# Kernel optimization log

Measured on AMD Instinct MI355X. Metric: run time of the kernel, lower is better.

## Reference

```python
import jax, jax.numpy as jnp
import numpy as np

N_EMBD = 1024
HEAD_SIZE = 64  # n_embd // n_head = 1024 // 16


def setup_inputs() -> dict:
    key = jax.random.key(0)
    ks = jax.random.split(key, 7)
    s = 0.02
    return {
        "x": jax.random.normal(ks[0], (8, 2048, N_EMBD), dtype=jnp.float32),
        "wq": jax.random.normal(ks[1], (N_EMBD, HEAD_SIZE), dtype=jnp.float32) * s,
        "bq": jax.random.normal(ks[2], (HEAD_SIZE,), dtype=jnp.float32) * s,
        "wk": jax.random.normal(ks[3], (N_EMBD, HEAD_SIZE), dtype=jnp.float32) * s,
        "bk": jax.random.normal(ks[4], (HEAD_SIZE,), dtype=jnp.float32) * s,
        "wv": jax.random.normal(ks[5], (N_EMBD, HEAD_SIZE), dtype=jnp.float32) * s,
        "bv": jax.random.normal(ks[6], (HEAD_SIZE,), dtype=jnp.float32) * s,
    }


def reference(x, wq, bq, wk, bk, wv, bv):
    B, T, C = x.shape
    q = x @ wq + bq  # [B,T,H]
    k = x @ wk + bk
    v = x @ wv + bv
    # NOTE: original scales by C**-0.5 where C = n_embd (full embedding dim)
    scale = jnp.asarray(C, x.dtype) ** -0.5
    att = jnp.einsum("bqh,bkh->bqk", q, k) * scale  # [B,T,T]
    causal = jnp.tril(jnp.ones((T, T), dtype=bool))
    att = jnp.where(causal, att, -jnp.inf)
    att = jax.nn.softmax(att, axis=-1)
    return jnp.einsum("bqk,bkh->bqh", att, v)  # [B,T,H]
```

## Files before the change

### kernel.cpp

```cpp
#include <hip/hip_runtime.h>
#include <hip/hip_bf16.h>

typedef short s8v __attribute__((ext_vector_type(8)));
typedef short s4v __attribute__((ext_vector_type(4)));
typedef float f4v __attribute__((ext_vector_type(4)));

#define MFMA16(a,b,c) __builtin_amdgcn_mfma_f32_16x16x32_bf16((a),(b),(c),0,0,0)

__device__ __forceinline__ short f2bf(float f) {
    __hip_bfloat16 h = __float2bfloat16(f);
    short s; __builtin_memcpy(&s, &h, 2); return s;
}
__device__ __forceinline__ float bf2f(short s) {
    unsigned int u = ((unsigned int)(unsigned short)s) << 16;
    float f; __builtin_memcpy(&f, &u, 4); return f;
}
__device__ __forceinline__ s4v cvt4(float4 a) {
    s4v r; r[0] = f2bf(a.x); r[1] = f2bf(a.y); r[2] = f2bf(a.z); r[3] = f2bf(a.w);
    return r;
}

__global__ __launch_bounds__(256) void pack_w_kernel(
    const float* __restrict__ wq, const float* __restrict__ wk,
    const float* __restrict__ wv, short* __restrict__ wpack)
{
    int fid  = blockIdx.x * 256 + threadIdx.x;
    int lane = fid & 63;
    int ks   = (fid >> 6) & 31;
    int t    = fid >> 11;
    int m3 = t >> 2, nt = t & 3;
    int col = nt * 16 + (lane & 15);
    int k0  = ks * 32 + (lane >> 4) * 8;
    const float* w = (m3 == 0) ? wq : (m3 == 1 ? wk : wv);
    float sc = (m3 == 0) ? 0.03125f : 1.0f;
    s8v frag;
#pragma unroll
    for (int j = 0; j < 8; j++) frag[j] = f2bf(w[(k0 + j) * 64 + col] * sc);
    ((s8v*)wpack)[fid] = frag;
}

__global__ __launch_bounds__(256) void qkv_kernel(
    const float* __restrict__ x, const short* __restrict__ wpack,
    const float* __restrict__ bq, const float* __restrict__ bk,
    const float* __restrict__ bv,
    short* __restrict__ qws, short* __restrict__ kws, short* __restrict__ vt)
{
    __shared__ short xl[2][32][136];

    int tid  = threadIdx.x;
    int wave = tid >> 6, lane = tid & 63;
    int quad = lane >> 4, l16 = lane & 15;
    int row0 = blockIdx.x * 32;
    const float* xbase = x + (size_t)row0 * 1024;
    const s8v* wp = (const s8v*)wpack;
    int tbase = wave * 3;

    f4v acc[2][3];
    f4v z = {0.f, 0.f, 0.f, 0.f};
#pragma unroll
    for (int rf = 0; rf < 2; rf++)
#pragma unroll
        for (int i = 0; i < 3; i++) acc[rf][i] = z;

    float4 xr[4];
#pragma unroll
    for (int i = 0; i < 4; i++) {
        int idx = i * 256 + tid;
        xr[i] = *(const float4*)(xbase + (size_t)(idx >> 5) * 1024 + (idx & 31) * 4);
    }
#pragma unroll
    for (int i = 0; i < 4; i++) {
        int idx = i * 256 + tid;
        *(s4v*)&xl[0][idx >> 5][(idx & 31) * 4] = cvt4(xr[i]);
    }
    __syncthreads();

    for (int sk = 0; sk < 8; sk++) {
        int cur = sk & 1, nxt = cur ^ 1;
        if (sk < 7) {
#pragma unroll
            for (int i = 0; i < 4; i++) {
                int idx = i * 256 + tid;
                xr[i] = *(const float4*)(xbase + (size_t)(idx >> 5) * 1024
                                         + (sk + 1) * 128 + (idx & 31) * 4);
            }
        }
#pragma unroll
        for (int ks = 0; ks < 4; ks++) {
            s8v a0 = *(const s8v*)&xl[cur][l16][ks * 32 + quad * 8];
            s8v a1 = *(const s8v*)&xl[cur][16 + l16][ks * 32 + quad * 8];
            int kg = sk * 4 + ks;
#pragma unroll
            for (int i = 0; i < 3; i++) {
                s8v bf = wp[((tbase + i) * 32 + kg) * 64 + lane];
                acc[0][i] = MFMA16(a0, bf, acc[0][i]);
                acc[1][i] = MFMA16(a1, bf, acc[1][i]);
            }
        }
        if (sk < 7) {
#pragma unroll
            for (int i = 0; i < 4; i++) {
                int idx = i * 256 + tid;
                *(s4v*)&xl[nxt][idx >> 5][(idx & 31) * 4] = cvt4(xr[i]);
            }
        }
        __syncthreads();
    }

    int b = row0 >> 11;
#pragma unroll
    for (int rf = 0; rf < 2; rf++) {
        int rowD = row0 + rf * 16 + quad * 4;
#pragma unroll
        for (int i = 0; i < 3; i++) {
            int t = tbase + i, m3 = t >> 2, nt = t & 3;
            int col = nt * 16 + l16;
            if (m3 == 0) {
                float bias = bq[col] * 0.03125f;
#pragma unroll
                for (int r = 0; r < 4; r++)
                    qws[(rowD + r) * 64 + col] = f2bf(acc[rf][i][r] + bias);
            } else if (m3 == 1) {
                float bias = bk[col];
#pragma unroll
                for (int r = 0; r < 4; r++)
                    kws[(rowD + r) * 64 + col] = f2bf(acc[rf][i][r] + bias);
            } else {
                float bias = bv[col];
                int keyb = rowD & 2047;
                s4v v4;
#pragma unroll
                for (int r = 0; r < 4; r++) v4[r] = f2bf(acc[rf][i][r] + bias);
                *(s4v*)(vt + (size_t)(b * 64 + col) * 2048 + keyb) = v4;
            }
        }
    }
}

__global__ __launch_bounds__(256) void attn_kernel(
    const short* __restrict__ qws, const short* __restrict__ kws,
    const short* __restrict__ vt, short* __restrict__ opart,
    float* __restrict__ lpart)
{
    __shared__ short Kl[64][72];
    __shared__ short Vl[64][72];
    __shared__ short Pl[4][16 * 72];

    int tid  = threadIdx.x;
    int wave = tid >> 6, lane = tid & 63;
    int quad = lane >> 4, l16 = lane & 15;
    int b = blockIdx.y;
    int u = 143 - blockIdx.x;

    int g = 0;
#pragma unroll
    for (int gg = 1; gg <= 7; gg++) if (u >= 2 * gg * (gg + 1)) g = gg;
    int rem = u - 2 * g * (g + 1);
    int qt = 4 * g + rem / (g + 1);
    int cc = rem % (g + 1);

    int q0 = qt * 64;
    int c0 = cc * 256;
    bool last = (cc == g);
    int jtN = last ? (((q0 + 63 - c0) >> 6) + 1) : 4;

    const short* qb  = qws + (size_t)b * 2048 * 64;
    const short* kb  = kws + (size_t)b * 2048 * 64;
    const short* vtb = vt  + (size_t)b * 64 * 2048;

    int qrow = q0 + wave * 16 + l16;
    s8v qf0 = *(const s8v*)(qb + qrow * 64 + quad * 8);
    s8v qf1 = *(const s8v*)(qb + qrow * 64 + 32 + quad * 8);

    s8v onef;
#pragma unroll
    for (int j = 0; j < 8; j++) onef[j] = (l16 == 0) ? (short)0x3F80 : (short)0;

    f4v o[5];
    f4v z = {0.f, 0.f, 0.f, 0.f};
#pragma unroll
    for (int nt = 0; nt < 5; nt++) o[nt] = z;

    int srow = tid >> 3;
    int sc   = (tid & 7) * 8;

    for (int t = 0; t < jtN; t++) {
        int key0 = c0 + t * 64;
        __syncthreads();
#pragma unroll
        for (int i = 0; i < 2; i++) {
            int r = srow + i * 32;
            *(s8v*)&Kl[r][sc] = *(const s8v*)(kb + (key0 + r) * 64 + sc);
            *(s8v*)&Vl[r][sc] = *(const s8v*)(vtb + (size_t)r * 2048 + key0 + sc);
        }
        __syncthreads();

        f4v s[4];
#pragma unroll
        for (int nt = 0; nt < 4; nt++) {
            s8v k0 = *(const s8v*)&Kl[nt * 16 + l16][quad * 8];
            s8v k1 = *(const s8v*)&Kl[nt * 16 + l16][32 + quad * 8];
            s[nt] = MFMA16(qf0, k0, z);
            s[nt] = MFMA16(qf1, k1, s[nt]);
        }

        if (last) {
            int rowbase = q0 + wave * 16 + quad * 4;
#pragma unroll
            for (int nt = 0; nt < 4; nt++) {
                int key = key0 + nt * 16 + l16;
#pragma unroll
                for (int r = 0; r < 4; r++)
                    if (key > rowbase + r) s[nt][r] = -1e30f;
            }
        }

        short* pw = Pl[wave];
#pragma unroll
        for (int nt = 0; nt < 4; nt++)
#pragma unroll
            for (int r = 0; r < 4; r++)
                pw[(quad * 4 + r) * 72 + nt * 16 + l16] = f2bf(__expf(s[nt][r]));
        asm volatile("s_waitcnt lgkmcnt(0)" ::: "memory");

#pragma unroll
        for (int st = 0; st < 2; st++) {
            s8v pf = *(const s8v*)(pw + l16 * 72 + st * 32 + quad * 8);
#pragma unroll
            for (int nt = 0; nt < 4; nt++) {
                s8v vf = *(const s8v*)&Vl[nt * 16 + l16][st * 32 + quad * 8];
                o[nt] = MFMA16(pf, vf, o[nt]);
            }
            o[4] = MFMA16(pf, onef, o[4]);
        }
    }

    int g0 = b * 2048 + q0 + wave * 16;
    short* op = opart + (size_t)cc * (16384 * 64);
#pragma unroll
    for (int nt = 0; nt < 4; nt++)
#pragma unroll
        for (int r = 0; r < 4; r++)
            op[(size_t)(g0 + quad * 4 + r) * 64 + nt * 16 + l16] = f2bf(o[nt][r]);
    if (l16 == 0) {
        float* lp = lpart + (size_t)cc * 16384;
#pragma unroll
        for (int r = 0; r < 4; r++) lp[g0 + quad * 4 + r] = o[4][r];
    }
}

__global__ __launch_bounds__(256) void combine_kernel(
    const short* __restrict__ opart, const float* __restrict__ lpart,
    float* __restrict__ out)
{
    int idx = blockIdx.x * 256 + threadIdx.x;
    int g = idx >> 4;
    int d = (idx & 15) * 4;
    int nc = ((g & 2047) >> 8) + 1;
    float s0 = 0.f, s1 = 0.f, s2 = 0.f, s3 = 0.f, lsum = 0.f;
    for (int c = 0; c < nc; c++) {
        short4 o4 = *(const short4*)(opart + (size_t)c * (16384 * 64) + g * 64 + d);
        s0 += bf2f(o4.x); s1 += bf2f(o4.y); s2 += bf2f(o4.z); s3 += bf2f(o4.w);
        lsum += lpart[c * 16384 + g];
    }
    float inv = 1.0f / lsum;
    float4 res = {s0 * inv, s1 * inv, s2 * inv, s3 * inv};
    *(float4*)(out + g * 64 + d) = res;
}

extern "C" void kernel_launch(void* const* d_in, const int* in_sizes, int n_in,
                              void* d_out, int out_size, void* d_ws, size_t ws_size,
                              hipStream_t stream) {
    const float* x  = (const float*)d_in[0];
    const float* wq = (const float*)d_in[1];
    const float* bq = (const float*)d_in[2];
    const float* wk = (const float*)d_in[3];
    const float* bk = (const float*)d_in[4];
    const float* wv = (const float*)d_in[5];
    const float* bv = (const float*)d_in[6];
    float* out = (float*)d_out;

    char* ws = (char*)d_ws;
    short* wpack = (short*)ws;
    short* qws   = (short*)(ws + (512u << 10));
    short* kws   = (short*)(ws + (512u << 10) + (2u << 20));
    short* vt    = (short*)(ws + (512u << 10) + (4u << 20));
    short* opart = (short*)(ws + (512u << 10) + (6u << 20));
    float* lpart = (float*)(ws + (512u << 10) + (22u << 20));

    hipLaunchKernelGGL(pack_w_kernel,  dim3(96),        dim3(256), 0, stream,
                       wq, wk, wv, wpack);
    hipLaunchKernelGGL(qkv_kernel,     dim3(512),       dim3(256), 0, stream,
                       x, wpack, bq, bk, bv, qws, kws, vt);
    hipLaunchKernelGGL(attn_kernel,    dim3(144, 8),    dim3(256), 0, stream,
                       qws, kws, vt, opart, lpart);
    hipLaunchKernelGGL(combine_kernel, dim3(1024),      dim3(256), 0, stream,
                       opart, lpart, out);
}
```

Measured before the change: 138.7 us.

## Double-buffer K/V tiles in attention and enlarge QKV projection row tiles

The attention kernel now prefetches the next K/V tile into registers while computing on the current shared-memory buffer, then writes it to a second buffer. This drops one barrier per iteration and hides global load latency. The QKV kernel moves to 512-thread blocks covering 64 rows with a narrower 64-wide k-step, so each weight fragment is reused across two row halves by different waves. The cost is more shared memory and registers, which may lower occupancy, and half as many QKV blocks.

```diff
diff --git a/kernel.cpp b/kernel.cpp
--- a/kernel.cpp
+++ b/kernel.cpp
@@ -39,21 +39,22 @@
     ((s8v*)wpack)[fid] = frag;
 }
 
-__global__ __launch_bounds__(256) void qkv_kernel(
+__global__ __launch_bounds__(512) void qkv_kernel(
     const float* __restrict__ x, const short* __restrict__ wpack,
     const float* __restrict__ bq, const float* __restrict__ bk,
     const float* __restrict__ bv,
     short* __restrict__ qws, short* __restrict__ kws, short* __restrict__ vt)
 {
-    __shared__ short xl[2][32][136];
+    __shared__ short xl[2][64][72];
 
     int tid  = threadIdx.x;
     int wave = tid >> 6, lane = tid & 63;
     int quad = lane >> 4, l16 = lane & 15;
-    int row0 = blockIdx.x * 32;
+    int row0 = blockIdx.x * 64;
+    int rhalf = (wave & 1) * 32;
+    int tbase = (wave >> 1) * 3;
     const float* xbase = x + (size_t)row0 * 1024;
     const s8v* wp = (const s8v*)wpack;
-    int tbase = wave * 3;
 
     f4v acc[2][3];
     f4v z = {0.f, 0.f, 0.f, 0.f};
@@ -62,34 +63,34 @@
 #pragma unroll
         for (int i = 0; i < 3; i++) acc[rf][i] = z;
 
-    float4 xr[4];
-#pragma unroll
-    for (int i = 0; i < 4; i++) {
-        int idx = i * 256 + tid;
-        xr[i] = *(const float4*)(xbase + (size_t)(idx >> 5) * 1024 + (idx & 31) * 4);
-    }
-#pragma unroll
-    for (int i = 0; i < 4; i++) {
-        int idx = i * 256 + tid;
-        *(s4v*)&xl[0][idx >> 5][(idx & 31) * 4] = cvt4(xr[i]);
+    float4 xr[2];
+#pragma unroll
+    for (int i = 0; i < 2; i++) {
+        int idx = i * 512 + tid;
+        xr[i] = *(const float4*)(xbase + (size_t)(idx >> 4) * 1024 + (idx & 15) * 4);
+    }
+#pragma unroll
+    for (int i = 0; i < 2; i++) {
+        int idx = i * 512 + tid;
+        *(s4v*)&xl[0][idx >> 4][(idx & 15) * 4] = cvt4(xr[i]);
     }
     __syncthreads();
 
-    for (int sk = 0; sk < 8; sk++) {
+    for (int sk = 0; sk < 16; sk++) {
         int cur = sk & 1, nxt = cur ^ 1;
-        if (sk < 7) {
-#pragma unroll
-            for (int i = 0; i < 4; i++) {
-                int idx = i * 256 + tid;
-                xr[i] = *(const float4*)(xbase + (size_t)(idx >> 5) * 1024
-                                         + (sk + 1) * 128 + (idx & 31) * 4);
-            }
-        }
-#pragma unroll
-        for (int ks = 0; ks < 4; ks++) {
-            s8v a0 = *(const s8v*)&xl[cur][l16][ks * 32 + quad * 8];
-            s8v a1 = *(const s8v*)&xl[cur][16 + l16][ks * 32 + quad * 8];
-            int kg = sk * 4 + ks;
+        if (sk < 15) {
+#pragma unroll
+            for (int i = 0; i < 2; i++) {
+                int idx = i * 512 + tid;
+                xr[i] = *(const float4*)(xbase + (size_t)(idx >> 4) * 1024
+                                         + (sk + 1) * 64 + (idx & 15) * 4);
+            }
+        }
+#pragma unroll
+        for (int ks = 0; ks < 2; ks++) {
+            s8v a0 = *(const s8v*)&xl[cur][rhalf + l16][ks * 32 + quad * 8];
+            s8v a1 = *(const s8v*)&xl[cur][rhalf + 16 + l16][ks * 32 + quad * 8];
+            int kg = sk * 2 + ks;
 #pragma unroll
             for (int i = 0; i < 3; i++) {
                 s8v bf = wp[((tbase + i) * 32 + kg) * 64 + lane];
@@ -97,20 +98,20 @@
                 acc[1][i] = MFMA16(a1, bf, acc[1][i]);
             }
         }
-        if (sk < 7) {
-#pragma unroll
-            for (int i = 0; i < 4; i++) {
-                int idx = i * 256 + tid;
-                *(s4v*)&xl[nxt][idx >> 5][(idx & 31) * 4] = cvt4(xr[i]);
-            }
-        }
-        __syncthreads();
+        if (sk < 15) {
+#pragma unroll
+            for (int i = 0; i < 2; i++) {
+                int idx = i * 512 + tid;
+                *(s4v*)&xl[nxt][idx >> 4][(idx & 15) * 4] = cvt4(xr[i]);
+            }
+            __syncthreads();
+        }
     }
 
     int b = row0 >> 11;
 #pragma unroll
     for (int rf = 0; rf < 2; rf++) {
-        int rowD = row0 + rf * 16 + quad * 4;
+        int rowD = row0 + rhalf + rf * 16 + quad * 4;
 #pragma unroll
         for (int i = 0; i < 3; i++) {
             int t = tbase + i, m3 = t >> 2, nt = t & 3;
@@ -142,8 +143,8 @@
     const short* __restrict__ vt, short* __restrict__ opart,
     float* __restrict__ lpart)
 {
-    __shared__ short Kl[64][72];
-    __shared__ short Vl[64][72];
+    __shared__ short Kl[2][64][72];
+    __shared__ short Vl[2][64][72];
     __shared__ short Pl[4][16 * 72];
 
     int tid  = threadIdx.x;
@@ -184,22 +185,41 @@
     int srow = tid >> 3;
     int sc   = (tid & 7) * 8;
 
+    s8v kr[2], vr[2];
+#pragma unroll
+    for (int i = 0; i < 2; i++) {
+        int r = srow + i * 32;
+        kr[i] = *(const s8v*)(kb + (c0 + r) * 64 + sc);
+        vr[i] = *(const s8v*)(vtb + (size_t)r * 2048 + c0 + sc);
+    }
+#pragma unroll
+    for (int i = 0; i < 2; i++) {
+        int r = srow + i * 32;
+        *(s8v*)&Kl[0][r][sc] = kr[i];
+        *(s8v*)&Vl[0][r][sc] = vr[i];
+    }
+    __syncthreads();
+
     for (int t = 0; t < jtN; t++) {
+        int cur = t & 1, nxt = cur ^ 1;
         int key0 = c0 + t * 64;
-        __syncthreads();
-#pragma unroll
-        for (int i = 0; i < 2; i++) {
-            int r = srow + i * 32;
-            *(s8v*)&Kl[r][sc] = *(const s8v*)(kb + (key0 + r) * 64 + sc);
-            *(s8v*)&Vl[r][sc] = *(const s8v*)(vtb + (size_t)r * 2048 + key0 + sc);
-        }
-        __syncthreads();
+        bool more = (t + 1 < jtN);
+
+        if (more) {
+            int key1 = key0 + 64;
+#pragma unroll
+            for (int i = 0; i < 2; i++) {
+                int r = srow + i * 32;
+                kr[i] = *(const s8v*)(kb + (key1 + r) * 64 + sc);
+                vr[i] = *(const s8v*)(vtb + (size_t)r * 2048 + key1 + sc);
+            }
+        }
 
         f4v s[4];
 #pragma unroll
         for (int nt = 0; nt < 4; nt++) {
-            s8v k0 = *(const s8v*)&Kl[nt * 16 + l16][quad * 8];
-            s8v k1 = *(const s8v*)&Kl[nt * 16 + l16][32 + quad * 8];
+            s8v k0 = *(const s8v*)&Kl[cur][nt * 16 + l16][quad * 8];
+            s8v k1 = *(const s8v*)&Kl[cur][nt * 16 + l16][32 + quad * 8];
             s[nt] = MFMA16(qf0, k0, z);
             s[nt] = MFMA16(qf1, k1, s[nt]);
         }
@@ -228,10 +248,20 @@
             s8v pf = *(const s8v*)(pw + l16 * 72 + st * 32 + quad * 8);
 #pragma unroll
             for (int nt = 0; nt < 4; nt++) {
-                s8v vf = *(const s8v*)&Vl[nt * 16 + l16][st * 32 + quad * 8];
+                s8v vf = *(const s8v*)&Vl[cur][nt * 16 + l16][st * 32 + quad * 8];
                 o[nt] = MFMA16(pf, vf, o[nt]);
             }
             o[4] = MFMA16(pf, onef, o[4]);
+        }
+
+        if (more) {
+#pragma unroll
+            for (int i = 0; i < 2; i++) {
+                int r = srow + i * 32;
+                *(s8v*)&Kl[nxt][r][sc] = kr[i];
+                *(s8v*)&Vl[nxt][r][sc] = vr[i];
+            }
+            __syncthreads();
         }
     }
 
@@ -290,7 +320,7 @@
 
     hipLaunchKernelGGL(pack_w_kernel,  dim3(96),        dim3(256), 0, stream,
                        wq, wk, wv, wpack);
-    hipLaunchKernelGGL(qkv_kernel,     dim3(512),       dim3(256), 0, stream,
+    hipLaunchKernelGGL(qkv_kernel,     dim3(256),       dim3(512), 0, stream,
                        x, wpack, bq, bk, bv, qws, kws, vt);
     hipLaunchKernelGGL(attn_kernel,    dim3(144, 8),    dim3(256), 0, stream,
                        qws, kws, vt, opart, lpart);
```

Result: slower. 143.0 us (+3.1%).

## Prefetch next K/V tile into registers and transpose S MFMA for packed P stores

Applied to the files above, without the earlier changes.

Loads for the next K/V tile are issued into registers right after the LDS store barrier, so global memory latency overlaps with the current tile's MFMA and softmax work. The QK^T MFMA operands are swapped so each lane holds four consecutive keys of one query row. That lets P be written to LDS as a single packed 8-byte store per tile instead of sixteen scalar 2-byte stores, with the causal mask indexing adjusted to match. The cost is extra registers for the prefetch buffers, which could reduce occupancy.

```diff
diff --git a/kernel.cpp b/kernel.cpp
--- a/kernel.cpp
+++ b/kernel.cpp
@@ -18,6 +18,10 @@
 __device__ __forceinline__ s4v cvt4(float4 a) {
     s4v r; r[0] = f2bf(a.x); r[1] = f2bf(a.y); r[2] = f2bf(a.z); r[3] = f2bf(a.w);
     return r;
+}
+__device__ __forceinline__ unsigned int pk2(float a, float b) {
+    return ((unsigned int)(unsigned short)f2bf(b) << 16) |
+           (unsigned int)(unsigned short)f2bf(a);
 }
 
 __global__ __launch_bounds__(256) void pack_w_kernel(
@@ -184,43 +188,65 @@
     int srow = tid >> 3;
     int sc   = (tid & 7) * 8;
 
+    s8v kr[2], vr[2];
+#pragma unroll
+    for (int i = 0; i < 2; i++) {
+        int r = srow + i * 32;
+        kr[i] = *(const s8v*)(kb + (c0 + r) * 64 + sc);
+        vr[i] = *(const s8v*)(vtb + (size_t)r * 2048 + c0 + sc);
+    }
+
     for (int t = 0; t < jtN; t++) {
         int key0 = c0 + t * 64;
+        bool more = (t + 1 < jtN);
+
         __syncthreads();
 #pragma unroll
         for (int i = 0; i < 2; i++) {
             int r = srow + i * 32;
-            *(s8v*)&Kl[r][sc] = *(const s8v*)(kb + (key0 + r) * 64 + sc);
-            *(s8v*)&Vl[r][sc] = *(const s8v*)(vtb + (size_t)r * 2048 + key0 + sc);
+            *(s8v*)&Kl[r][sc] = kr[i];
+            *(s8v*)&Vl[r][sc] = vr[i];
         }
         __syncthreads();
+
+        if (more) {
+            int key1 = key0 + 64;
+#pragma unroll
+            for (int i = 0; i < 2; i++) {
+                int r = srow + i * 32;
+                kr[i] = *(const s8v*)(kb + (key1 + r) * 64 + sc);
+                vr[i] = *(const s8v*)(vtb + (size_t)r * 2048 + key1 + sc);
+            }
+        }
 
         f4v s[4];
 #pragma unroll
         for (int nt = 0; nt < 4; nt++) {
             s8v k0 = *(const s8v*)&Kl[nt * 16 + l16][quad * 8];
             s8v k1 = *(const s8v*)&Kl[nt * 16 + l16][32 + quad * 8];
-            s[nt] = MFMA16(qf0, k0, z);
-            s[nt] = MFMA16(qf1, k1, s[nt]);
+            s[nt] = MFMA16(k0, qf0, z);
+            s[nt] = MFMA16(k1, qf1, s[nt]);
         }
 
         if (last) {
-            int rowbase = q0 + wave * 16 + quad * 4;
+            int qg = q0 + wave * 16 + l16;
 #pragma unroll
             for (int nt = 0; nt < 4; nt++) {
-                int key = key0 + nt * 16 + l16;
+                int keyb = key0 + nt * 16 + quad * 4;
 #pragma unroll
                 for (int r = 0; r < 4; r++)
-                    if (key > rowbase + r) s[nt][r] = -1e30f;
+                    if (keyb + r > qg) s[nt][r] = -1e30f;
             }
         }
 
         short* pw = Pl[wave];
 #pragma unroll
-        for (int nt = 0; nt < 4; nt++)
-#pragma unroll
-            for (int r = 0; r < 4; r++)
-                pw[(quad * 4 + r) * 72 + nt * 16 + l16] = f2bf(__expf(s[nt][r]));
+        for (int nt = 0; nt < 4; nt++) {
+            uint2 d;
+            d.x = pk2(__expf(s[nt][0]), __expf(s[nt][1]));
+            d.y = pk2(__expf(s[nt][2]), __expf(s[nt][3]));
+            *(uint2*)&pw[l16 * 72 + nt * 16 + quad * 4] = d;
+        }
         asm volatile("s_waitcnt lgkmcnt(0)" ::: "memory");
 
 #pragma unroll
```

After: 134.8 us. -2.8%, faster.
